# Performance work log

Hardware: AMD Instinct MI355X
Metric: run time of the kernel (lower is better)

## Reference

```python
import jax, jax.numpy as jnp
import numpy as np

N = 2048
D_T = 256; D_F = 256
E_T = 32; E_F = 32; E_C = 128
C = 5; Q = 512


def setup_inputs() -> dict:
    key = jax.random.key(0)
    ks = jax.random.split(key, 12)
    # full graph minus self-loops, row-major (matches dense_to_sparse ordering)
    r, c = np.meshgrid(np.arange(N), np.arange(N), indexing='ij')
    m = r != c
    edge_index = jnp.asarray(np.stack([r[m], c[m]]), dtype=jnp.int32)  # [2, N*(N-1)]
    E = edge_index.shape[1]
    s = 0.02
    return {
        'time_features': jax.random.normal(ks[0], (N, D_T), jnp.float32),
        'edge_index': edge_index,
        'time_edge_weight': jax.random.uniform(ks[1], (E,), jnp.float32),
        'freq_features': jax.random.normal(ks[2], (N, D_F), jnp.float32),
        'freq_edge_weight': jax.random.uniform(ks[3], (E,), jnp.float32),
        'labels': jax.random.randint(ks[4], (N,), 0, C, jnp.int32),
        'num_classes': C,
        'query_size': Q,
        'Wt': jax.random.normal(ks[5], (D_T, E_T), jnp.float32) * s,
        'bt': jnp.zeros((E_T,), jnp.float32),
        'Wf': jax.random.normal(ks[6], (D_F, E_F), jnp.float32) * s,
        'bf': jnp.zeros((E_F,), jnp.float32),
        'Wc': jax.random.normal(ks[7], (E_T + E_F + C, E_C), jnp.float32) * s,
        'bc': jnp.zeros((E_C,), jnp.float32),
        'Wo': jax.random.normal(ks[8], (E_C, C), jnp.float32) * s,
        'bo': jnp.zeros((C,), jnp.float32),
    }


def _gcn(x, A, W, b):
    # torch_geometric GCNConv: D^{-1/2}(A + I)D^{-1/2} (X W) + b
    n = A.shape[0]
    Ah = A + jnp.eye(n, dtype=A.dtype)
    deg = Ah.sum(axis=1)
    dis = jnp.where(deg > 0, jax.lax.rsqrt(deg), 0.0)
    return (dis[:, None] * Ah * dis[None, :]) @ (x @ W) + b


def reference(time_features, edge_index, time_edge_weight, freq_features,
              freq_edge_weight, labels, num_classes, query_size,
              Wt, bt, Wf, bf, Wc, bc, Wo, bo):
    n = time_features.shape[0]
    lrelu = lambda z: jax.nn.leaky_relu(z, 0.01)

    def dense_adj(w):  # A[dst, src] = w
        return jnp.zeros((n, n), w.dtype).at[edge_index[1], edge_index[0]].add(w)

    te = lrelu(_gcn(time_features, dense_adj(time_edge_weight), Wt, bt))
    fe = lrelu(_gcn(freq_features, dense_adj(freq_edge_weight), Wf, bf))

    # to_one_hot: one_hot[:n - query_size, labels] = 1 -> support rows get 1 in
    # every column that appears anywhere in `labels`
    cols = jnp.zeros((num_classes,), te.dtype).at[labels].set(1.0)
    rowmask = (jnp.arange(n) < (n - query_size)).astype(te.dtype)
    one_hot = rowmask[:, None] * cols[None, :]

    feats = jnp.concatenate([te, fe, one_hot], axis=-1)  # [n, E_T+E_F+C]

    # graph_construction (no_grad in original): 1 / (L1 distance over the
    # non-one-hot dims + 1e-5), zero diagonal
    fd = jax.lax.stop_gradient(feats[:, : feats.shape[1] - num_classes])
    dist = jnp.sum(jnp.abs(fd[:, None, :] - fd[None, :, :]), axis=-1)  # [n, n]
    Aw = (1.0 / (dist + 1e-5)) * (1.0 - jnp.eye(n, dtype=feats.dtype))

    emb = lrelu(_gcn(feats, Aw, Wc, bc))
    return emb @ Wo + bo
```

## Files before the change

### kernel.cpp

```cpp
#include <hip/hip_runtime.h>
#include <hip/hip_bf16.h>

#define N 2048
#define NM1 2047
#define DT 256
#define ET 32
#define EC 128
#define NC 5
#define FS 80
#define FD 69
#define KC_ET 16
#define KC_EC 8

typedef __hip_bfloat16 bf16;

__global__ __launch_bounds__(256) void k_deg(const float* __restrict__ tw,
                                             const float* __restrict__ fw,
                                             float* __restrict__ degT,
                                             float* __restrict__ degF){
    int p = blockIdx.x*256 + threadIdx.x;
    if (p >= NM1) return;
    int s0 = blockIdx.y*32;
    float lowT=0.f, highT=0.f, lowF=0.f, highF=0.f;
    #pragma unroll 8
    for (int r = 0; r < 32; ++r){
        int s = s0 + r;
        float vt = tw[(size_t)s*NM1 + p];
        float vf = fw[(size_t)s*NM1 + p];
        if (s <= p){ highT += vt; highF += vf; }
        else       { lowT  += vt; lowF  += vf; }
    }
    atomicAdd(&degT[p],   lowT);
    atomicAdd(&degF[p],   lowF);
    atomicAdd(&degT[p+1], highT);
    atomicAdd(&degF[p+1], highF);
}

__global__ void k_labelmask(const int* __restrict__ labels, float* __restrict__ cols){
    __shared__ float lc[NC];
    int t = threadIdx.x;
    if (t < NC) lc[t] = 0.f;
    __syncthreads();
    for (int i = t; i < N; i += 256){
        int l = labels[i];
        if (l >= 0 && l < NC) lc[l] = 1.f;
    }
    __syncthreads();
    if (t < NC) cols[t] = lc[t];
}

__global__ __launch_bounds__(256) void k_xw_scale(const float* __restrict__ X,
                                                  const float* __restrict__ W,
                                                  const float* __restrict__ deg,
                                                  float* __restrict__ Z){
    __shared__ float Ws[DT*ET];
    __shared__ float Xs[8*DT];
    int t = threadIdx.x;
    for (int idx = t; idx < DT*ET; idx += 256) Ws[idx] = W[idx];
    int i0 = blockIdx.x*8;
    for (int idx = t; idx < 8*DT; idx += 256) Xs[idx] = X[(size_t)i0*DT + idx];
    __syncthreads();
    int r = t >> 5, f = t & 31;
    const float* xr = Xs + r*DT;
    float acc = 0.f;
    #pragma unroll 8
    for (int d = 0; d < DT; ++d) acc += xr[d]*Ws[d*ET+f];
    int i = i0 + r;
    Z[(size_t)i*ET+f] = rsqrtf(1.f + deg[i])*acc;
}

__global__ __launch_bounds__(256) void k_agg_et(const float* __restrict__ tw,
                                                const float* __restrict__ fw,
                                                const float* __restrict__ Zt,
                                                const float* __restrict__ Zf,
                                                float* __restrict__ Pt,
                                                float* __restrict__ Pf){
    __shared__ float Ast[64*68];
    __shared__ float Asf[64*68];
    __shared__ float Zst[64*ET];
    __shared__ float Zsf[64*ET];
    int t = threadIdx.x;
    int i0 = blockIdx.x*64;
    int kc = blockIdx.y;
    int k0 = kc*128;
    int lane_i = t & 63;
    int krow0  = (t >> 6)*16;
    int gi = i0 + lane_i;
    int tf = t & 31;
    int tr = t >> 5;
    float accT[8], accF[8];
    #pragma unroll
    for (int u = 0; u < 8; ++u){ accT[u]=0.f; accF[u]=0.f; }

    for (int kt = 0; kt < 2; ++kt){
        int kb = k0 + kt*64;
        #pragma unroll 4
        for (int e = 0; e < 16; ++e){
            int kl = krow0 + e;
            int k  = kb + kl;
            float vt, vf;
            if (gi == k){ vt = 0.f; vf = 0.f; }
            else {
                size_t base = (size_t)k*NM1 + gi - (gi > k ? 1 : 0);
                vt = tw[base]; vf = fw[base];
            }
            Ast[kl*68 + lane_i] = vt;
            Asf[kl*68 + lane_i] = vf;
        }
        #pragma unroll
        for (int h = 0; h < 2; ++h){
            int id = t + h*256;
            int row = id >> 3;
            int c4  = (id & 7)*4;
            *(float4*)&Zst[row*ET + c4] = *(const float4*)&Zt[(size_t)(kb+row)*ET + c4];
            *(float4*)&Zsf[row*ET + c4] = *(const float4*)&Zf[(size_t)(kb+row)*ET + c4];
        }
        __syncthreads();
        for (int k = 0; k < 64; ++k){
            float zt = Zst[k*ET + tf];
            float zf = Zsf[k*ET + tf];
            const float* at = &Ast[k*68 + tr*8];
            const float* af = &Asf[k*68 + tr*8];
            float4 a0 = *(const float4*)(at);
            float4 a1 = *(const float4*)(at+4);
            float4 b0 = *(const float4*)(af);
            float4 b1 = *(const float4*)(af+4);
            accT[0]+=a0.x*zt; accT[1]+=a0.y*zt; accT[2]+=a0.z*zt; accT[3]+=a0.w*zt;
            accT[4]+=a1.x*zt; accT[5]+=a1.y*zt; accT[6]+=a1.z*zt; accT[7]+=a1.w*zt;
            accF[0]+=b0.x*zf; accF[1]+=b0.y*zf; accF[2]+=b0.z*zf; accF[3]+=b0.w*zf;
            accF[4]+=b1.x*zf; accF[5]+=b1.y*zf; accF[6]+=b1.z*zf; accF[7]+=b1.w*zf;
        }
        __syncthreads();
    }
    #pragma unroll
    for (int u = 0; u < 8; ++u){
        size_t ii = (size_t)(i0 + tr*8 + u);
        Pt[(size_t)kc*(N*ET) + ii*ET + tf] = accT[u];
        Pf[(size_t)kc*(N*ET) + ii*ET + tf] = accF[u];
    }
}

__global__ __launch_bounds__(256) void k_feats_epi(const float* __restrict__ Pt,
                                                   const float* __restrict__ Pf,
                                                   const float* __restrict__ Zt,
                                                   const float* __restrict__ Zf,
                                                   const float* __restrict__ degT,
                                                   const float* __restrict__ degF,
                                                   const float* __restrict__ bt,
                                                   const float* __restrict__ bfv,
                                                   const float* __restrict__ cols,
                                                   const int* __restrict__ qsize,
                                                   float* __restrict__ feats){
    int idx = blockIdx.x*256 + threadIdx.x;
    int i = idx >> 6;
    int f = idx & 63;
    float s, rd, b;
    if (f < ET){
        s = Zt[(size_t)i*ET + f];
        #pragma unroll
        for (int kc = 0; kc < KC_ET; ++kc) s += Pt[(size_t)kc*(N*ET) + (size_t)i*ET + f];
        rd = rsqrtf(1.f + degT[i]);
        b = bt[f];
    } else {
        int g = f - ET;
        s = Zf[(size_t)i*ET + g];
        #pragma unroll
        for (int kc = 0; kc < KC_ET; ++kc) s += Pf[(size_t)kc*(N*ET) + (size_t)i*ET + g];
        rd = rsqrtf(1.f + degF[i]);
        b = bfv[g];
    }
    float v = rd*s + b;
    feats[(size_t)i*FS + f] = v > 0.f ? v : 0.01f*v;
    if (f < NC){
        int nsup = N - qsize[0];
        feats[(size_t)i*FS + 2*ET + f] = (i < nsup) ? cols[f] : 0.f;
    }
}

__global__ __launch_bounds__(256) void k_build_aw(const float* __restrict__ feats,
                                                  float* __restrict__ Aw){
    __shared__ float fi[64*65];
    __shared__ float fj[64*65];
    int t = threadIdx.x;
    int i0 = blockIdx.x*64, j0 = blockIdx.y*64;
    {
        int row = t >> 2;
        int seg = (t & 3) * 16;
        const float4* si = (const float4*)(feats + (size_t)(i0+row)*FS + seg);
        const float4* sj = (const float4*)(feats + (size_t)(j0+row)*FS + seg);
        #pragma unroll
        for (int s = 0; s < 4; ++s){
            float4 v = si[s];
            float4 w = sj[s];
            int c = seg + s*4;
            fi[row*65+c+0]=v.x; fi[row*65+c+1]=v.y; fi[row*65+c+2]=v.z; fi[row*65+c+3]=v.w;
            fj[row*65+c+0]=w.x; fj[row*65+c+1]=w.y; fj[row*65+c+2]=w.z; fj[row*65+c+3]=w.w;
        }
    }
    __syncthreads();
    int tx = t & 15, ty = t >> 4;
    float acc[4][4];
    #pragma unroll
    for (int u=0;u<4;++u)
        #pragma unroll
        for (int v=0;v<4;++v) acc[u][v]=0.f;
    for (int k = 0; k < 64; ++k){
        float a0 = fi[(ty*4+0)*65+k], a1 = fi[(ty*4+1)*65+k];
        float a2 = fi[(ty*4+2)*65+k], a3 = fi[(ty*4+3)*65+k];
        float b0 = fj[(tx*4+0)*65+k], b1 = fj[(tx*4+1)*65+k];
        float b2 = fj[(tx*4+2)*65+k], b3 = fj[(tx*4+3)*65+k];
        acc[0][0]+=fabsf(a0-b0); acc[0][1]+=fabsf(a0-b1); acc[0][2]+=fabsf(a0-b2); acc[0][3]+=fabsf(a0-b3);
        acc[1][0]+=fabsf(a1-b0); acc[1][1]+=fabsf(a1-b1); acc[1][2]+=fabsf(a1-b2); acc[1][3]+=fabsf(a1-b3);
        acc[2][0]+=fabsf(a2-b0); acc[2][1]+=fabsf(a2-b1); acc[2][2]+=fabsf(a2-b2); acc[2][3]+=fabsf(a2-b3);
        acc[3][0]+=fabsf(a3-b0); acc[3][1]+=fabsf(a3-b1); acc[3][2]+=fabsf(a3-b2); acc[3][3]+=fabsf(a3-b3);
    }
    #pragma unroll
    for (int u = 0; u < 4; ++u){
        int gi = i0 + ty*4 + u;
        float4 o;
        float* po = (float*)&o;
        #pragma unroll
        for (int v = 0; v < 4; ++v){
            int gj = j0 + tx*4 + v;
            po[v] = (gi==gj) ? 1.0f : 1.0f/(acc[u][v] + 1e-5f);
        }
        *(float4*)(Aw + (size_t)gi*N + j0 + tx*4) = o;
    }
}

__global__ __launch_bounds__(256) void k_row_rsqrt(const float* __restrict__ A,
                                                   float* __restrict__ dis){
    int row = blockIdx.x;
    const float4* Ar = (const float4*)(A + (size_t)row*N);
    float s = 0.f;
    for (int i = threadIdx.x; i < N/4; i += 256){
        float4 v = Ar[i];
        s += (v.x+v.y)+(v.z+v.w);
    }
    #pragma unroll
    for (int off = 32; off > 0; off >>= 1) s += __shfl_xor(s, off, 64);
    __shared__ float red[4];
    int wid = threadIdx.x >> 6;
    if ((threadIdx.x & 63) == 0) red[wid] = s;
    __syncthreads();
    if (threadIdx.x == 0){
        float deg = red[0]+red[1]+red[2]+red[3];
        dis[row] = (deg > 0.f) ? 1.0f/sqrtf(deg) : 0.f;
    }
}

__global__ __launch_bounds__(256) void k_featswc(const float* __restrict__ feats,
                                                 const float* __restrict__ Wc,
                                                 const float* __restrict__ disw,
                                                 float* __restrict__ Zc){
    __shared__ float Wcs[FD*EC];
    __shared__ float fr[8][FD+3];
    int t = threadIdx.x;
    for (int idx = t; idx < FD*EC; idx += 256) Wcs[idx] = Wc[idx];
    int i0 = blockIdx.x*8;
    for (int idx = t; idx < 8*FD; idx += 256){
        int r = idx / FD;
        int c = idx - r*FD;
        fr[r][c] = feats[(size_t)(i0+r)*FS + c];
    }
    __syncthreads();
    int f  = t & 127;
    int rh = t >> 7;
    for (int rr = 0; rr < 4; ++rr){
        int r = rh*4 + rr;
        float acc = 0.f;
        #pragma unroll
        for (int d = 0; d < FD; ++d) acc += fr[r][d]*Wcs[d*EC+f];
        int i = i0 + r;
        Zc[(size_t)i*EC + f] = disw[i]*acc;
    }
}

__global__ __launch_bounds__(256) void k_agg_ec(const float* __restrict__ Aw,
                                                const float* __restrict__ Zc,
                                                float* __restrict__ Pe){
    __shared__ float Aws[32*65];
    __shared__ float Zcs[64*EC];
    int t = threadIdx.x;
    int i0 = blockIdx.x*32;
    int kc = blockIdx.y;
    int k0 = kc*256;
    int tf = t & 31, tr = t >> 5;
    int f0 = tf*4;
    float acc[4][4];
    #pragma unroll
    for (int v=0;v<4;++v)
        #pragma unroll
        for (int u=0;u<4;++u) acc[v][u]=0.f;

    for (int kt = 0; kt < 4; ++kt){
        int kb = k0 + kt*64;
        #pragma unroll
        for (int h = 0; h < 2; ++h){
            int id = t + h*256;
            int row = id >> 4;
            int c4  = (id & 15)*4;
            float4 v = *(const float4*)&Aw[(size_t)(i0+row)*N + kb + c4];
            Aws[row*65 + c4 + 0] = v.x;
            Aws[row*65 + c4 + 1] = v.y;
            Aws[row*65 + c4 + 2] = v.z;
            Aws[row*65 + c4 + 3] = v.w;
        }
        #pragma unroll
        for (int h = 0; h < 8; ++h){
            int id = t + h*256;
            int row = id >> 5;
            int c4  = (id & 31)*4;
            *(float4*)&Zcs[row*EC + c4] = *(const float4*)&Zc[(size_t)(kb+row)*EC + c4];
        }
        __syncthreads();
        for (int k = 0; k < 64; ++k){
            float4 z = *(const float4*)&Zcs[k*EC + f0];
            float a0 = Aws[(tr*4+0)*65 + k];
            float a1 = Aws[(tr*4+1)*65 + k];
            float a2 = Aws[(tr*4+2)*65 + k];
            float a3 = Aws[(tr*4+3)*65 + k];
            acc[0][0]+=a0*z.x; acc[0][1]+=a0*z.y; acc[0][2]+=a0*z.z; acc[0][3]+=a0*z.w;
            acc[1][0]+=a1*z.x; acc[1][1]+=a1*z.y; acc[1][2]+=a1*z.z; acc[1][3]+=a1*z.w;
            acc[2][0]+=a2*z.x; acc[2][1]+=a2*z.y; acc[2][2]+=a2*z.z; acc[2][3]+=a2*z.w;
            acc[3][0]+=a3*z.x; acc[3][1]+=a3*z.y; acc[3][2]+=a3*z.z; acc[3][3]+=a3*z.w;
        }
        __syncthreads();
    }
    #pragma unroll
    for (int v = 0; v < 4; ++v){
        size_t ii = (size_t)(i0 + tr*4 + v);
        float4 o; o.x=acc[v][0]; o.y=acc[v][1]; o.z=acc[v][2]; o.w=acc[v][3];
        *(float4*)&Pe[(size_t)kc*(N*EC) + ii*EC + f0] = o;
    }
}

__global__ __launch_bounds__(256) void k_emb_epi(const float* __restrict__ Pe,
                                                 const float* __restrict__ disw,
                                                 const float* __restrict__ bc,
                                                 float* __restrict__ emb){
    int idx = blockIdx.x*256 + threadIdx.x;
    int i = idx >> 7, f = idx & 127;
    float s = 0.f;
    #pragma unroll
    for (int kc = 0; kc < KC_EC; ++kc) s += Pe[(size_t)kc*(N*EC) + (size_t)idx];
    float v = disw[i]*s + bc[f];
    emb[idx] = v > 0.f ? v : 0.01f*v;
}

__global__ __launch_bounds__(256) void k_final(const float* __restrict__ emb,
                                               const float* __restrict__ Wo,
                                               const float* __restrict__ bo,
                                               float* __restrict__ out){
    __shared__ float Wos[EC*NC];
    __shared__ float bos[NC];
    int t = threadIdx.x;
    for (int idx = t; idx < EC*NC; idx += 256) Wos[idx] = Wo[idx];
    if (t < NC) bos[t] = bo[t];
    __syncthreads();
    int idx = blockIdx.x*256 + t;
    int i = idx / NC;
    int c = idx - i*NC;
    float acc = bos[c];
    const float* er = emb + (size_t)i*EC;
    #pragma unroll 8
    for (int f = 0; f < EC; ++f) acc += er[f]*Wos[f*NC+c];
    out[idx] = acc;
}

extern "C" void kernel_launch(void* const* d_in, const int* in_sizes, int n_in,
                              void* d_out, int out_size, void* d_ws, size_t ws_size,
                              hipStream_t stream) {
    const float* time_features = (const float*)d_in[0];
    const float* tw            = (const float*)d_in[2];
    const float* freq_features = (const float*)d_in[3];
    const float* fw            = (const float*)d_in[4];
    const int*   labels        = (const int*)d_in[5];
    const int*   qsize         = (const int*)d_in[7];
    const float* Wt  = (const float*)d_in[8];
    const float* bt  = (const float*)d_in[9];
    const float* Wf  = (const float*)d_in[10];
    const float* bfv = (const float*)d_in[11];
    const float* Wc  = (const float*)d_in[12];
    const float* bc  = (const float*)d_in[13];
    const float* Wo  = (const float*)d_in[14];
    const float* bo  = (const float*)d_in[15];
    float* out = (float*)d_out;

    float* ws    = (float*)d_ws;
    float* Zt    = ws;
    float* Zf    = Zt + (size_t)N*ET;
    float* Zc    = Zf + (size_t)N*ET;
    float* degT  = Zc + (size_t)N*EC;
    float* degF  = degT + N;
    float* disw  = degF + N;
    float* colsb = disw + N;
    float* feats = colsb + 8;
    float* emb   = feats + (size_t)N*FS;
    float* Aw    = emb + (size_t)N*EC;
    float* Pt    = Aw + (size_t)N*N;
    float* Pf    = Pt + (size_t)KC_ET*N*ET;
    float* Pe    = Pf + (size_t)KC_ET*N*ET;

    hipMemsetAsync(degT, 0, 2*N*sizeof(float), stream);
    k_deg<<<dim3(8, 64), 256, 0, stream>>>(tw, fw, degT, degF);
    k_labelmask<<<1, 256, 0, stream>>>(labels, colsb);
    k_xw_scale<<<N/8, 256, 0, stream>>>(time_features, Wt, degT, Zt);
    k_xw_scale<<<N/8, 256, 0, stream>>>(freq_features, Wf, degF, Zf);
    k_agg_et<<<dim3(N/64, KC_ET), 256, 0, stream>>>(tw, fw, Zt, Zf, Pt, Pf);
    k_feats_epi<<<(N*64)/256, 256, 0, stream>>>(Pt, Pf, Zt, Zf, degT, degF,
                                                bt, bfv, colsb, qsize, feats);
    k_build_aw<<<dim3(N/64, N/64), 256, 0, stream>>>(feats, Aw);
    k_row_rsqrt<<<N, 256, 0, stream>>>(Aw, disw);
    k_featswc<<<N/8, 256, 0, stream>>>(feats, Wc, disw, Zc);
    k_agg_ec<<<dim3(N/32, KC_EC), 256, 0, stream>>>(Aw, Zc, Pe);
    k_emb_epi<<<(N*EC)/256, 256, 0, stream>>>(Pe, disw, bc, emb);
    k_final<<<(N*NC)/256, 256, 0, stream>>>(emb, Wo, bo, out);
}
```

Before: 230.5 us.

## Fuse small launches, fold row-degree into Aw build, retile aggregation GEMMs

```diff
diff --git a/kernel.cpp b/kernel.cpp
--- a/kernel.cpp
+++ b/kernel.cpp
@@ -10,17 +10,33 @@
 #define FS 80
 #define FD 69
 #define KC_ET 16
-#define KC_EC 8
+#define KC_EC 16
 
 typedef __hip_bfloat16 bf16;
 
-__global__ __launch_bounds__(256) void k_deg(const float* __restrict__ tw,
-                                             const float* __restrict__ fw,
-                                             float* __restrict__ degT,
-                                             float* __restrict__ degF){
-    int p = blockIdx.x*256 + threadIdx.x;
+__global__ __launch_bounds__(256) void k_deg_label(const float* __restrict__ tw,
+                                                   const float* __restrict__ fw,
+                                                   const int* __restrict__ labels,
+                                                   float* __restrict__ degT,
+                                                   float* __restrict__ degF,
+                                                   float* __restrict__ cols){
+    int b = blockIdx.x;
+    int t = threadIdx.x;
+    if (b == 512){
+        __shared__ float lc[NC];
+        if (t < NC) lc[t] = 0.f;
+        __syncthreads();
+        for (int i = t; i < N; i += 256){
+            int l = labels[i];
+            if (l >= 0 && l < NC) lc[l] = 1.f;
+        }
+        __syncthreads();
+        if (t < NC) cols[t] = lc[t];
+        return;
+    }
+    int p = (b & 7)*256 + t;
     if (p >= NM1) return;
-    int s0 = blockIdx.y*32;
+    int s0 = (b >> 3)*32;
     float lowT=0.f, highT=0.f, lowF=0.f, highF=0.f;
     #pragma unroll 8
     for (int r = 0; r < 32; ++r){
@@ -36,23 +52,18 @@
     atomicAdd(&degF[p+1], highF);
 }
 
-__global__ void k_labelmask(const int* __restrict__ labels, float* __restrict__ cols){
-    __shared__ float lc[NC];
-    int t = threadIdx.x;
-    if (t < NC) lc[t] = 0.f;
-    __syncthreads();
-    for (int i = t; i < N; i += 256){
-        int l = labels[i];
-        if (l >= 0 && l < NC) lc[l] = 1.f;
-    }
-    __syncthreads();
-    if (t < NC) cols[t] = lc[t];
-}
-
-__global__ __launch_bounds__(256) void k_xw_scale(const float* __restrict__ X,
-                                                  const float* __restrict__ W,
-                                                  const float* __restrict__ deg,
-                                                  float* __restrict__ Z){
+__global__ __launch_bounds__(256) void k_xw2(const float* __restrict__ Xt,
+                                             const float* __restrict__ Wt,
+                                             const float* __restrict__ degT,
+                                             float* __restrict__ Zt,
+                                             const float* __restrict__ Xf,
+                                             const float* __restrict__ Wf,
+                                             const float* __restrict__ degF,
+                                             float* __restrict__ Zf){
+    const float* X   = blockIdx.y ? Xf   : Xt;
+    const float* W   = blockIdx.y ? Wf   : Wt;
+    const float* deg = blockIdx.y ? degF : degT;
+    float*       Z   = blockIdx.y ? Zf   : Zt;
     __shared__ float Ws[DT*ET];
     __shared__ float Xs[8*DT];
     int t = threadIdx.x;
@@ -69,7 +80,7 @@
     Z[(size_t)i*ET+f] = rsqrtf(1.f + deg[i])*acc;
 }
 
-__global__ __launch_bounds__(256) void k_agg_et(const float* __restrict__ tw,
+__global__ __launch_bounds__(128) void k_agg_et(const float* __restrict__ tw,
                                                 const float* __restrict__ fw,
                                                 const float* __restrict__ Zt,
                                                 const float* __restrict__ Zf,
@@ -83,33 +94,35 @@
     int i0 = blockIdx.x*64;
     int kc = blockIdx.y;
     int k0 = kc*128;
-    int lane_i = t & 63;
-    int krow0  = (t >> 6)*16;
-    int gi = i0 + lane_i;
-    int tf = t & 31;
-    int tr = t >> 5;
-    float accT[8], accF[8];
-    #pragma unroll
-    for (int u = 0; u < 8; ++u){ accT[u]=0.f; accF[u]=0.f; }
+    int rowg = t >> 3;
+    int colth = t & 7;
+    int r0 = rowg*4, c0 = colth*4;
+    float accT[4][4], accF[4][4];
+    #pragma unroll
+    for (int u=0;u<4;++u)
+        #pragma unroll
+        for (int v=0;v<4;++v){ accT[u][v]=0.f; accF[u][v]=0.f; }
 
     for (int kt = 0; kt < 2; ++kt){
         int kb = k0 + kt*64;
-        #pragma unroll 4
-        for (int e = 0; e < 16; ++e){
-            int kl = krow0 + e;
-            int k  = kb + kl;
+        #pragma unroll
+        for (int e = 0; e < 32; ++e){
+            int id = t + e*128;
+            int k_l = id >> 6, i_l = id & 63;
+            int k = kb + k_l;
+            int gi = i0 + i_l;
             float vt, vf;
             if (gi == k){ vt = 0.f; vf = 0.f; }
             else {
                 size_t base = (size_t)k*NM1 + gi - (gi > k ? 1 : 0);
                 vt = tw[base]; vf = fw[base];
             }
-            Ast[kl*68 + lane_i] = vt;
-            Asf[kl*68 + lane_i] = vf;
-        }
-        #pragma unroll
-        for (int h = 0; h < 2; ++h){
-            int id = t + h*256;
+            Ast[k_l*68 + i_l] = vt;
+            Asf[k_l*68 + i_l] = vf;
+        }
+        #pragma unroll
+        for (int e = 0; e < 4; ++e){
+            int id = t + e*128;
             int row = id >> 3;
             int c4  = (id & 7)*4;
             *(float4*)&Zst[row*ET + c4] = *(const float4*)&Zt[(size_t)(kb+row)*ET + c4];
@@ -117,26 +130,33 @@
         }
         __syncthreads();
         for (int k = 0; k < 64; ++k){
-            float zt = Zst[k*ET + tf];
-            float zf = Zsf[k*ET + tf];
-            const float* at = &Ast[k*68 + tr*8];
-            const float* af = &Asf[k*68 + tr*8];
-            float4 a0 = *(const float4*)(at);
-            float4 a1 = *(const float4*)(at+4);
-            float4 b0 = *(const float4*)(af);
-            float4 b1 = *(const float4*)(af+4);
-            accT[0]+=a0.x*zt; accT[1]+=a0.y*zt; accT[2]+=a0.z*zt; accT[3]+=a0.w*zt;
-            accT[4]+=a1.x*zt; accT[5]+=a1.y*zt; accT[6]+=a1.z*zt; accT[7]+=a1.w*zt;
-            accF[0]+=b0.x*zf; accF[1]+=b0.y*zf; accF[2]+=b0.z*zf; accF[3]+=b0.w*zf;
-            accF[4]+=b1.x*zf; accF[5]+=b1.y*zf; accF[6]+=b1.z*zf; accF[7]+=b1.w*zf;
-        }
-        __syncthreads();
-    }
-    #pragma unroll
-    for (int u = 0; u < 8; ++u){
-        size_t ii = (size_t)(i0 + tr*8 + u);
-        Pt[(size_t)kc*(N*ET) + ii*ET + tf] = accT[u];
-        Pf[(size_t)kc*(N*ET) + ii*ET + tf] = accF[u];
+            float4 at = *(const float4*)&Ast[k*68 + r0];
+            float4 af = *(const float4*)&Asf[k*68 + r0];
+            float4 zt = *(const float4*)&Zst[k*ET + c0];
+            float4 zf = *(const float4*)&Zsf[k*ET + c0];
+            const float* ap = (const float*)&at;
+            const float* bp = (const float*)&af;
+            const float* zp = (const float*)&zt;
+            const float* wp = (const float*)&zf;
+            #pragma unroll
+            for (int u = 0; u < 4; ++u)
+                #pragma unroll
+                for (int v = 0; v < 4; ++v){
+                    accT[u][v] += ap[u]*zp[v];
+                    accF[u][v] += bp[u]*wp[v];
+                }
+        }
+        __syncthreads();
+    }
+    #pragma unroll
+    for (int u = 0; u < 4; ++u){
+        size_t ii = (size_t)(i0 + r0 + u);
+        float4 ot, of;
+        float* pt = (float*)&ot; float* pf = (float*)&of;
+        #pragma unroll
+        for (int v = 0; v < 4; ++v){ pt[v]=accT[u][v]; pf[v]=accF[u][v]; }
+        *(float4*)&Pt[(size_t)kc*(N*ET) + ii*ET + c0] = ot;
+        *(float4*)&Pf[(size_t)kc*(N*ET) + ii*ET + c0] = of;
     }
 }
 
@@ -178,23 +198,24 @@
 }
 
 __global__ __launch_bounds__(256) void k_build_aw(const float* __restrict__ feats,
-                                                  float* __restrict__ Aw){
-    __shared__ float fi[64*65];
-    __shared__ float fj[64*65];
+                                                  float* __restrict__ Aw,
+                                                  float* __restrict__ dsum){
+    __shared__ float fiT[64*68];
+    __shared__ float fjT[64*68];
     int t = threadIdx.x;
     int i0 = blockIdx.x*64, j0 = blockIdx.y*64;
     {
         int row = t >> 2;
-        int seg = (t & 3) * 16;
-        const float4* si = (const float4*)(feats + (size_t)(i0+row)*FS + seg);
-        const float4* sj = (const float4*)(feats + (size_t)(j0+row)*FS + seg);
+        int cb  = (t & 3)*16;
+        const float4* si = (const float4*)(feats + (size_t)(i0+row)*FS + cb);
+        const float4* sj = (const float4*)(feats + (size_t)(j0+row)*FS + cb);
         #pragma unroll
         for (int s = 0; s < 4; ++s){
             float4 v = si[s];
             float4 w = sj[s];
-            int c = seg + s*4;
-            fi[row*65+c+0]=v.x; fi[row*65+c+1]=v.y; fi[row*65+c+2]=v.z; fi[row*65+c+3]=v.w;
-            fj[row*65+c+0]=w.x; fj[row*65+c+1]=w.y; fj[row*65+c+2]=w.z; fj[row*65+c+3]=w.w;
+            int c = cb + s*4;
+            fiT[(c+0)*68+row]=v.x; fiT[(c+1)*68+row]=v.y; fiT[(c+2)*68+row]=v.z; fiT[(c+3)*68+row]=v.w;
+            fjT[(c+0)*68+row]=w.x; fjT[(c+1)*68+row]=w.y; fjT[(c+2)*68+row]=w.z; fjT[(c+3)*68+row]=w.w;
         }
     }
     __syncthreads();
@@ -204,15 +225,16 @@
     for (int u=0;u<4;++u)
         #pragma unroll
         for (int v=0;v<4;++v) acc[u][v]=0.f;
-    for (int k = 0; k < 64; ++k){
-        float a0 = fi[(ty*4+0)*65+k], a1 = fi[(ty*4+1)*65+k];
-        float a2 = fi[(ty*4+2)*65+k], a3 = fi[(ty*4+3)*65+k];
-        float b0 = fj[(tx*4+0)*65+k], b1 = fj[(tx*4+1)*65+k];
-        float b2 = fj[(tx*4+2)*65+k], b3 = fj[(tx*4+3)*65+k];
-        acc[0][0]+=fabsf(a0-b0); acc[0][1]+=fabsf(a0-b1); acc[0][2]+=fabsf(a0-b2); acc[0][3]+=fabsf(a0-b3);
-        acc[1][0]+=fabsf(a1-b0); acc[1][1]+=fabsf(a1-b1); acc[1][2]+=fabsf(a1-b2); acc[1][3]+=fabsf(a1-b3);
-        acc[2][0]+=fabsf(a2-b0); acc[2][1]+=fabsf(a2-b1); acc[2][2]+=fabsf(a2-b2); acc[2][3]+=fabsf(a2-b3);
-        acc[3][0]+=fabsf(a3-b0); acc[3][1]+=fabsf(a3-b1); acc[3][2]+=fabsf(a3-b2); acc[3][3]+=fabsf(a3-b3);
+    for (int d = 0; d < 64; ++d){
+        float4 a4 = *(const float4*)&fiT[d*68 + ty*4];
+        float4 b4 = *(const float4*)&fjT[d*68 + tx*4];
+        const float* ap = (const float*)&a4;
+        const float* bp = (const float*)&b4;
+        #pragma unroll
+        for (int u = 0; u < 4; ++u)
+            #pragma unroll
+            for (int v = 0; v < 4; ++v)
+                acc[u][v] += fabsf(ap[u]-bp[v]);
     }
     #pragma unroll
     for (int u = 0; u < 4; ++u){
@@ -224,34 +246,19 @@
             int gj = j0 + tx*4 + v;
             po[v] = (gi==gj) ? 1.0f : 1.0f/(acc[u][v] + 1e-5f);
         }
-        *(float4*)(Aw + (size_t)gi*N + j0 + tx*4) = o;
-    }
-}
-
-__global__ __launch_bounds__(256) void k_row_rsqrt(const float* __restrict__ A,
-                                                   float* __restrict__ dis){
-    int row = blockIdx.x;
-    const float4* Ar = (const float4*)(A + (size_t)row*N);
-    float s = 0.f;
-    for (int i = threadIdx.x; i < N/4; i += 256){
-        float4 v = Ar[i];
-        s += (v.x+v.y)+(v.z+v.w);
-    }
-    #pragma unroll
-    for (int off = 32; off > 0; off >>= 1) s += __shfl_xor(s, off, 64);
-    __shared__ float red[4];
-    int wid = threadIdx.x >> 6;
-    if ((threadIdx.x & 63) == 0) red[wid] = s;
-    __syncthreads();
-    if (threadIdx.x == 0){
-        float deg = red[0]+red[1]+red[2]+red[3];
-        dis[row] = (deg > 0.f) ? 1.0f/sqrtf(deg) : 0.f;
+        *(float4*)&Aw[(size_t)gi*N + j0 + tx*4] = o;
+        float rs = (po[0]+po[1]) + (po[2]+po[3]);
+        rs += __shfl_xor(rs, 1);
+        rs += __shfl_xor(rs, 2);
+        rs += __shfl_xor(rs, 4);
+        rs += __shfl_xor(rs, 8);
+        if (tx == 0) atomicAdd(&dsum[gi], rs);
     }
 }
 
 __global__ __launch_bounds__(256) void k_featswc(const float* __restrict__ feats,
                                                  const float* __restrict__ Wc,
-                                                 const float* __restrict__ disw,
+                                                 const float* __restrict__ dsum,
                                                  float* __restrict__ Zc){
     __shared__ float Wcs[FD*EC];
     __shared__ float fr[8][FD+3];
@@ -272,71 +279,77 @@
         #pragma unroll
         for (int d = 0; d < FD; ++d) acc += fr[r][d]*Wcs[d*EC+f];
         int i = i0 + r;
-        Zc[(size_t)i*EC + f] = disw[i]*acc;
-    }
-}
-
-__global__ __launch_bounds__(256) void k_agg_ec(const float* __restrict__ Aw,
+        Zc[(size_t)i*EC + f] = rsqrtf(dsum[i])*acc;
+    }
+}
+
+__global__ __launch_bounds__(128) void k_agg_ec(const float* __restrict__ Aw,
                                                 const float* __restrict__ Zc,
                                                 float* __restrict__ Pe){
-    __shared__ float Aws[32*65];
-    __shared__ float Zcs[64*EC];
-    int t = threadIdx.x;
-    int i0 = blockIdx.x*32;
+    __shared__ float AwT[64*68];
+    __shared__ float Zs[64*132];
+    int t = threadIdx.x;
+    int i0 = blockIdx.x*64;
     int kc = blockIdx.y;
-    int k0 = kc*256;
-    int tf = t & 31, tr = t >> 5;
-    int f0 = tf*4;
-    float acc[4][4];
-    #pragma unroll
-    for (int v=0;v<4;++v)
-        #pragma unroll
-        for (int u=0;u<4;++u) acc[v][u]=0.f;
-
-    for (int kt = 0; kt < 4; ++kt){
+    int k0 = kc*128;
+    int colth = t & 15, rowg = t >> 4;
+    int r0 = rowg*8, c0 = colth*8;
+    float acc[8][8];
+    #pragma unroll
+    for (int u=0;u<8;++u)
+        #pragma unroll
+        for (int v=0;v<8;++v) acc[u][v]=0.f;
+
+    for (int kt = 0; kt < 2; ++kt){
         int kb = k0 + kt*64;
         #pragma unroll
-        for (int h = 0; h < 2; ++h){
-            int id = t + h*256;
-            int row = id >> 4;
-            int c4  = (id & 15)*4;
-            float4 v = *(const float4*)&Aw[(size_t)(i0+row)*N + kb + c4];
-            Aws[row*65 + c4 + 0] = v.x;
-            Aws[row*65 + c4 + 1] = v.y;
-            Aws[row*65 + c4 + 2] = v.z;
-            Aws[row*65 + c4 + 3] = v.w;
-        }
-        #pragma unroll
-        for (int h = 0; h < 8; ++h){
-            int id = t + h*256;
+        for (int e = 0; e < 8; ++e){
+            int id = t + e*128;
+            int i_l = id >> 4;
+            int k4  = (id & 15)*4;
+            float4 v = *(const float4*)&Aw[(size_t)(i0+i_l)*N + kb + k4];
+            AwT[(k4+0)*68 + i_l] = v.x;
+            AwT[(k4+1)*68 + i_l] = v.y;
+            AwT[(k4+2)*68 + i_l] = v.z;
+            AwT[(k4+3)*68 + i_l] = v.w;
+        }
+        #pragma unroll
+        for (int e = 0; e < 16; ++e){
+            int id = t + e*128;
             int row = id >> 5;
             int c4  = (id & 31)*4;
-            *(float4*)&Zcs[row*EC + c4] = *(const float4*)&Zc[(size_t)(kb+row)*EC + c4];
+            *(float4*)&Zs[row*132 + c4] = *(const float4*)&Zc[(size_t)(kb+row)*EC + c4];
         }
         __syncthreads();
         for (int k = 0; k < 64; ++k){
-            float4 z = *(const float4*)&Zcs[k*EC + f0];
-            float a0 = Aws[(tr*4+0)*65 + k];
-            float a1 = Aws[(tr*4+1)*65 + k];
-            float a2 = Aws[(tr*4+2)*65 + k];
-            float a3 = Aws[(tr*4+3)*65 + k];
-            acc[0][0]+=a0*z.x; acc[0][1]+=a0*z.y; acc[0][2]+=a0*z.z; acc[0][3]+=a0*z.w;
-            acc[1][0]+=a1*z.x; acc[1][1]+=a1*z.y; acc[1][2]+=a1*z.z; acc[1][3]+=a1*z.w;
-            acc[2][0]+=a2*z.x; acc[2][1]+=a2*z.y; acc[2][2]+=a2*z.z; acc[2][3]+=a2*z.w;
-            acc[3][0]+=a3*z.x; acc[3][1]+=a3*z.y; acc[3][2]+=a3*z.z; acc[3][3]+=a3*z.w;
-        }
-        __syncthreads();
-    }
-    #pragma unroll
-    for (int v = 0; v < 4; ++v){
-        size_t ii = (size_t)(i0 + tr*4 + v);
-        float4 o; o.x=acc[v][0]; o.y=acc[v][1]; o.z=acc[v][2]; o.w=acc[v][3];
-        *(float4*)&Pe[(size_t)kc*(N*EC) + ii*EC + f0] = o;
+            float4 alo = *(const float4*)&AwT[k*68 + r0];
+            float4 ahi = *(const float4*)&AwT[k*68 + r0 + 4];
+            float4 zlo = *(const float4*)&Zs[k*132 + c0];
+            float4 zhi = *(const float4*)&Zs[k*132 + c0 + 4];
+            float a8[8] = {alo.x,alo.y,alo.z,alo.w,ahi.x,ahi.y,ahi.z,ahi.w};
+            float z8[8] = {zlo.x,zlo.y,zlo.z,zlo.w,zhi.x,zhi.y,zhi.z,zhi.w};
+            #pragma unroll
+            for (int u = 0; u < 8; ++u)
+                #pragma unroll
+                for (int v = 0; v < 8; ++v)
+                    acc[u][v] += a8[u]*z8[v];
+        }
+        __syncthreads();
+    }
+    #pragma unroll
+    for (int u = 0; u < 8; ++u){
+        size_t ii = (size_t)(i0 + r0 + u);
+        float4 o0, o1;
+        float* p0 = (float*)&o0; float* p1 = (float*)&o1;
+        #pragma unroll
+        for (int v = 0; v < 4; ++v){ p0[v]=acc[u][v]; p1[v]=acc[u][v+4]; }
+        *(float4*)&Pe[(size_t)kc*(N*EC) + ii*EC + c0]     = o0;
+        *(float4*)&Pe[(size_t)kc*(N*EC) + ii*EC + c0 + 4] = o1;
     }
 }
 
 __global__ __launch_bounds__(256) void k_emb_epi(const float* __restrict__ Pe,
-                                                 const float* __restrict__ disw,
+                                                 const float* __restrict__ dsum,
                                                  const float* __restrict__ bc,
                                                  float* __restrict__ emb){
     int idx = blockIdx.x*256 + threadIdx.x;
@@ -344,7 +357,7 @@
     float s = 0.f;
     #pragma unroll
     for (int kc = 0; kc < KC_EC; ++kc) s += Pe[(size_t)kc*(N*EC) + (size_t)idx];
-    float v = disw[i]*s + bc[f];
+    float v = rsqrtf(dsum[i])*s + bc[f];
     emb[idx] = v > 0.f ? v : 0.01f*v;
 }
 
@@ -393,8 +406,8 @@
     float* Zc    = Zf + (size_t)N*ET;
     float* degT  = Zc + (size_t)N*EC;
     float* degF  = degT + N;
-    float* disw  = degF + N;
-    float* colsb = disw + N;
+    float* dsum  = degF + N;
+    float* colsb = dsum + N;
     float* feats = colsb + 8;
     float* emb   = feats + (size_t)N*FS;
     float* Aw    = emb + (size_t)N*EC;
@@ -402,18 +415,16 @@
     float* Pf    = Pt + (size_t)KC_ET*N*ET;
     float* Pe    = Pf + (size_t)KC_ET*N*ET;
 
-    hipMemsetAsync(degT, 0, 2*N*sizeof(float), stream);
-    k_deg<<<dim3(8, 64), 256, 0, stream>>>(tw, fw, degT, degF);
-    k_labelmask<<<1, 256, 0, stream>>>(labels, colsb);
-    k_xw_scale<<<N/8, 256, 0, stream>>>(time_features, Wt, degT, Zt);
-    k_xw_scale<<<N/8, 256, 0, stream>>>(freq_features, Wf, degF, Zf);
-    k_agg_et<<<dim3(N/64, KC_ET), 256, 0, stream>>>(tw, fw, Zt, Zf, Pt, Pf);
+    hipMemsetAsync(degT, 0, 3*N*sizeof(float), stream);
+    k_deg_label<<<513, 256, 0, stream>>>(tw, fw, labels, degT, degF, colsb);
+    k_xw2<<<dim3(N/8, 2), 256, 0, stream>>>(time_features, Wt, degT, Zt,
+                                            freq_features, Wf, degF, Zf);
+    k_agg_et<<<dim3(N/64, KC_ET), 128, 0, stream>>>(tw, fw, Zt, Zf, Pt, Pf);
     k_feats_epi<<<(N*64)/256, 256, 0, stream>>>(Pt, Pf, Zt, Zf, degT, degF,
                                                 bt, bfv, colsb, qsize, feats);
-    k_build_aw<<<dim3(N/64, N/64), 256, 0, stream>>>(feats, Aw);
-    k_row_rsqrt<<<N, 256, 0, stream>>>(Aw, disw);
-    k_featswc<<<N/8, 256, 0, stream>>>(feats, Wc, disw, Zc);
-    k_agg_ec<<<dim3(N/32, KC_EC), 256, 0, stream>>>(Aw, Zc, Pe);
-    k_emb_epi<<<(N*EC)/256, 256, 0, stream>>>(Pe, disw, bc, emb);
+    k_build_aw<<<dim3(N/64, N/64), 256, 0, stream>>>(feats, Aw, dsum);
+    k_featswc<<<N/8, 256, 0, stream>>>(feats, Wc, dsum, Zc);
+    k_agg_ec<<<dim3(N/64, KC_EC), 128, 0, stream>>>(Aw, Zc, Pe);
+    k_emb_epi<<<(N*EC)/256, 256, 0, stream>>>(Pe, dsum, bc, emb);
     k_final<<<(N*NC)/256, 256, 0, stream>>>(emb, Wo, bo, out);
 }
```

New measurement: 236.6 us. +2.7%, slower.
